# Optimization experiments

Hardware: AMD Instinct MI355X
Metric: run time of the kernel (lower is better)

Reference implementation:

```python
import jax, jax.numpy as jnp
import numpy as np

B, V, E, L, D = 16, 19, 361, 256, 64  # batch, vertices, edges/graph, seq_len, d_model
F_IN = 2 * D + 1  # concat(src_feat, tgt_feat, edge_weight)


def _linear_init(key, fan_in, fan_out):
    bound = 1.0 / np.sqrt(fan_in)
    kw, kb = jax.random.split(key)
    W = jax.random.uniform(kw, (fan_in, fan_out), jnp.float32, -bound, bound)
    b = jax.random.uniform(kb, (fan_out,), jnp.float32, -bound, bound)
    return W, b


def setup_inputs() -> dict:
    key = jax.random.key(0)
    ks = jax.random.split(key, 6)
    hidden_states = jax.random.normal(ks[0], (B * V, L, D), jnp.float32)
    edge_index = jax.random.randint(ks[1], (2, B * E, L), 0, B * V, dtype=jnp.int32)
    edge_weight = jax.random.uniform(ks[2], (B * E, L), jnp.float32)
    W1, b1 = _linear_init(ks[3], F_IN, D)
    W2, b2 = _linear_init(ks[4], D, D // 2)
    W3, b3 = _linear_init(ks[5], D // 2, 1)
    skip_param = jnp.float32(0.25)
    return {"hidden_states": hidden_states, "edge_weight": edge_weight,
            "W1": W1, "b1": b1, "W2": W2, "b2": b2, "W3": W3, "b3": b3,
            "skip_param": skip_param, "edge_index": edge_index}


def reference(hidden_states, edge_weight, W1, b1, W2, b2, W3, b3, skip_param, edge_index):
    # hidden_states: (B*V, L, D) -> (B, L, V, D) for per-timestep node gather
    hs = hidden_states.reshape(B, V, L, D).transpose(0, 2, 1, 3)
    # edge indices are global node ids; local vertex id = idx % V (as in torch code)
    src = (edge_index[0] % V).reshape(B, E, L).transpose(0, 2, 1)  # (B, L, E)
    tgt = (edge_index[1] % V).reshape(B, E, L).transpose(0, 2, 1)
    ew = edge_weight.reshape(B, E, L).transpose(0, 2, 1)           # (B, L, E)
    src_feat = jnp.take_along_axis(hs, src[..., None], axis=2)    # (B, L, E, D)
    tgt_feat = jnp.take_along_axis(hs, tgt[..., None], axis=2)    # (B, L, E, D)
    x = jnp.concatenate([src_feat, tgt_feat, ew[..., None]], axis=-1)  # (B, L, E, 2D+1)
    h = jax.nn.silu(x @ W1 + b1)
    h = jax.nn.silu(h @ W2 + b2)
    w = jax.nn.sigmoid((h @ W3 + b3)[..., 0])                     # (B, L, E)
    new_ew = skip_param * ew + (1.0 - skip_param) * w
    return new_ew.transpose(0, 2, 1).reshape(B * E, L)            # (B*E, L)
```

## Files before the change

### kernel.cpp

```cpp
#include <hip/hip_runtime.h>

#define NB 16
#define NV 19
#define NE 361
#define NL 256
#define ND 64
#define NT 23
#define NEP (NT * 16)
#define ASTRIDE 136

typedef __attribute__((ext_vector_type(8))) short bf16x8;
typedef __attribute__((ext_vector_type(4))) float f32x4;
typedef __attribute__((ext_vector_type(2))) __bf16 bf16v2;

union bf8u { unsigned u[4]; bf16x8 v; uint4 q; };

__device__ __forceinline__ unsigned pack_bf16(float lo, float hi) {
    bf16v2 v; v.x = (__bf16)lo; v.y = (__bf16)hi;
    return __builtin_bit_cast(unsigned, v);
}
__device__ __forceinline__ short f2bf(float f) {
    __bf16 h = (__bf16)f;
    return __builtin_bit_cast(short, h);
}
__device__ __forceinline__ float bflo(unsigned u) {
    return __builtin_bit_cast(float, u << 16);
}
__device__ __forceinline__ float bfhi(unsigned u) {
    return __builtin_bit_cast(float, u & 0xffff0000u);
}
__device__ __forceinline__ f32x4 silu4(f32x4 x) {
    f32x4 t = x * -1.44269504f;
    f32x4 d;
    d.x = __builtin_amdgcn_exp2f(t.x);
    d.y = __builtin_amdgcn_exp2f(t.y);
    d.z = __builtin_amdgcn_exp2f(t.z);
    d.w = __builtin_amdgcn_exp2f(t.w);
    d += 1.f;
    f32x4 r;
    r.x = __builtin_amdgcn_rcpf(d.x);
    r.y = __builtin_amdgcn_rcpf(d.y);
    r.z = __builtin_amdgcn_rcpf(d.z);
    r.w = __builtin_amdgcn_rcpf(d.w);
    return x * r;
}
__device__ __forceinline__ float sigm(float x) {
    return __builtin_amdgcn_rcpf(1.f + __builtin_amdgcn_exp2f(x * -1.44269504f));
}

__global__ __launch_bounds__(256, 4) void edge_learner_kernel(
    const float* __restrict__ hs,
    const float* __restrict__ ew_in,
    const float* __restrict__ W1,
    const float* __restrict__ b1,
    const float* __restrict__ W2,
    const float* __restrict__ b2,
    const float* __restrict__ W3,
    const float* __restrict__ b3,
    const float* __restrict__ skip_p,
    const int*   __restrict__ eidx,
    float* __restrict__ out)
{
    __shared__ __align__(16) short A_s[NV * ASTRIDE];
    __shared__ __align__(16) int4  meta_s[NEP];

    const int tid  = threadIdx.x;
    const int lane = tid & 63;
    const int wave = tid >> 6;
    const int lq   = lane >> 4;
    const int lm   = lane & 15;
    const int bid0 = blockIdx.x;
    const int bid  = (bid0 & 7) * 512 + (bid0 >> 3);
    const int b    = bid >> 8;
    const int l    = bid & 255;

    for (int e = tid; e < NEP; e += 256) {
        int4 m;
        if (e < NE) {
            size_t row = (size_t)(b * NE + e) * NL + l;
            m.x = (eidx[row] % NV) * ASTRIDE;
            m.y = (eidx[(size_t)NB * NE * NL + row] % NV) * ASTRIDE + 64;
            m.z = __builtin_bit_cast(int, ew_in[row]);
            m.w = 0;
        } else {
            m.x = 0; m.y = 64; m.z = 0; m.w = 0;
        }
        meta_s[e] = m;
    }

    f32x4 w1lv[2][2], b1v[2][2];
    #pragma unroll
    for (int ks = 0; ks < 2; ++ks) {
        w1lv[ks][0] = *(const f32x4*)&W1[128 * 64 + ks * 32 + lq * 8];
        w1lv[ks][1] = *(const f32x4*)&W1[128 * 64 + ks * 32 + lq * 8 + 4];
        b1v[ks][0]  = *(const f32x4*)&b1[ks * 32 + lq * 8];
        b1v[ks][1]  = *(const f32x4*)&b1[ks * 32 + lq * 8 + 4];
    }
    bf8u w2f[2][2];
    #pragma unroll
    for (int nt = 0; nt < 2; ++nt)
        #pragma unroll
        for (int ks = 0; ks < 2; ++ks) {
            const float* w2p = &W2[(ks * 32 + lq * 8) * 32 + nt * 16 + lm];
            #pragma unroll
            for (int p = 0; p < 4; ++p)
                w2f[nt][ks].u[p] = pack_bf16(w2p[(2 * p) * 32], w2p[(2 * p + 1) * 32]);
        }
    const f32x4 b2v0 = *(const f32x4*)&b2[lq * 4];
    const f32x4 b2v1 = *(const f32x4*)&b2[16 + lq * 4];
    const f32x4 w3v0 = *(const f32x4*)&W3[lq * 4];
    const f32x4 w3v1 = *(const f32x4*)&W3[16 + lq * 4];
    const float b3v  = b3[0];
    const float skip = skip_p[0];

    {
        const int half = wave >> 1;
        const int oc0  = (wave & 1) * 32;
        bf8u w1f[2][2];
        #pragma unroll
        for (int nt = 0; nt < 2; ++nt)
            #pragma unroll
            for (int ks = 0; ks < 2; ++ks) {
                const float* wp = &W1[(half * 64 + ks * 32 + lq * 8) * 64
                                      + oc0 + nt * 16 + lm];
                #pragma unroll
                for (int p = 0; p < 4; ++p)
                    w1f[nt][ks].u[p] = pack_bf16(wp[(2 * p) * 64], wp[(2 * p + 1) * 64]);
            }

        f32x4 acc00 = {0,0,0,0}, acc01 = {0,0,0,0}, acc10 = {0,0,0,0}, acc11 = {0,0,0,0};
        #pragma unroll
        for (int Mt = 0; Mt < 2; ++Mt) {
            int v  = Mt * 16 + lm;
            int vc = v < NV ? v : NV - 1;
            const float* hp = hs + ((size_t)(b * NV + vc) * NL + l) * ND;
            bf8u af[2];
            #pragma unroll
            for (int ks = 0; ks < 2; ++ks) {
                float4 x0 = *(const float4*)&hp[ks * 32 + lq * 8];
                float4 x1 = *(const float4*)&hp[ks * 32 + lq * 8 + 4];
                af[ks].u[0] = pack_bf16(x0.x, x0.y);
                af[ks].u[1] = pack_bf16(x0.z, x0.w);
                af[ks].u[2] = pack_bf16(x1.x, x1.y);
                af[ks].u[3] = pack_bf16(x1.z, x1.w);
            }
            if (Mt == 0) {
                acc00 = __builtin_amdgcn_mfma_f32_16x16x32_bf16(af[0].v, w1f[0][0].v, acc00, 0, 0, 0);
                acc00 = __builtin_amdgcn_mfma_f32_16x16x32_bf16(af[1].v, w1f[0][1].v, acc00, 0, 0, 0);
                acc01 = __builtin_amdgcn_mfma_f32_16x16x32_bf16(af[0].v, w1f[1][0].v, acc01, 0, 0, 0);
                acc01 = __builtin_amdgcn_mfma_f32_16x16x32_bf16(af[1].v, w1f[1][1].v, acc01, 0, 0, 0);
            } else {
                acc10 = __builtin_amdgcn_mfma_f32_16x16x32_bf16(af[0].v, w1f[0][0].v, acc10, 0, 0, 0);
                acc10 = __builtin_amdgcn_mfma_f32_16x16x32_bf16(af[1].v, w1f[0][1].v, acc10, 0, 0, 0);
                acc11 = __builtin_amdgcn_mfma_f32_16x16x32_bf16(af[0].v, w1f[1][0].v, acc11, 0, 0, 0);
                acc11 = __builtin_amdgcn_mfma_f32_16x16x32_bf16(af[1].v, w1f[1][1].v, acc11, 0, 0, 0);
            }
        }
        #pragma unroll
        for (int r = 0; r < 4; ++r) {
            int v0 = lq * 4 + r;
            A_s[v0 * ASTRIDE + wave * 32 + lm]      = f2bf(acc00[r]);
            A_s[v0 * ASTRIDE + wave * 32 + 16 + lm] = f2bf(acc01[r]);
            int v1 = 16 + lq * 4 + r;
            if (v1 < NV) {
                A_s[v1 * ASTRIDE + wave * 32 + lm]      = f2bf(acc10[r]);
                A_s[v1 * ASTRIDE + wave * 32 + 16 + lm] = f2bf(acc11[r]);
            }
        }
    }
    __syncthreads();

    for (int t = wave; t < NT; t += 4) {
        const int ebase = t * 16;
        const int4 m  = meta_s[ebase + lm];
        const int  so = m.x;
        const int  to = m.y;
        const float ew = __builtin_bit_cast(float, m.z);

        bf8u a1[2];
        #pragma unroll
        for (int ks = 0; ks < 2; ++ks) {
            uint4 as = *(const uint4*)&A_s[so + ks * 32 + lq * 8];
            uint4 at = *(const uint4*)&A_s[to + ks * 32 + lq * 8];
            f32x4 x0, x1;
            x0.x = bflo(as.x) + bflo(at.x);
            x0.y = bfhi(as.x) + bfhi(at.x);
            x0.z = bflo(as.y) + bflo(at.y);
            x0.w = bfhi(as.y) + bfhi(at.y);
            x1.x = bflo(as.z) + bflo(at.z);
            x1.y = bfhi(as.z) + bfhi(at.z);
            x1.z = bflo(as.w) + bflo(at.w);
            x1.w = bfhi(as.w) + bfhi(at.w);
            x0 += b1v[ks][0];  x0 += ew * w1lv[ks][0];
            x1 += b1v[ks][1];  x1 += ew * w1lv[ks][1];
            f32x4 y0 = silu4(x0);
            f32x4 y1 = silu4(x1);
            a1[ks].u[0] = pack_bf16(y0.x, y0.y);
            a1[ks].u[1] = pack_bf16(y0.z, y0.w);
            a1[ks].u[2] = pack_bf16(y1.x, y1.y);
            a1[ks].u[3] = pack_bf16(y1.z, y1.w);
        }

        f32x4 c0 = {0,0,0,0}, c1 = {0,0,0,0};
        c0 = __builtin_amdgcn_mfma_f32_16x16x32_bf16(w2f[0][0].v, a1[0].v, c0, 0, 0, 0);
        c0 = __builtin_amdgcn_mfma_f32_16x16x32_bf16(w2f[0][1].v, a1[1].v, c0, 0, 0, 0);
        c1 = __builtin_amdgcn_mfma_f32_16x16x32_bf16(w2f[1][0].v, a1[0].v, c1, 0, 0, 0);
        c1 = __builtin_amdgcn_mfma_f32_16x16x32_bf16(w2f[1][1].v, a1[1].v, c1, 0, 0, 0);

        f32x4 h0 = silu4(c0 + b2v0);
        f32x4 h1 = silu4(c1 + b2v1);
        f32x4 pv = h0 * w3v0 + h1 * w3v1;
        float p  = (pv.x + pv.y) + (pv.z + pv.w);
        p += __shfl_xor(p, 16);
        p += __shfl_xor(p, 32);

        if (lane < 16) {
            int er = ebase + lane;
            if (er < NE) {
                float wgt = sigm(p + b3v);
                out[(size_t)(b * NE + er) * NL + l] = skip * ew + (1.f - skip) * wgt;
            }
        }
    }
}

extern "C" void kernel_launch(void* const* d_in, const int* in_sizes, int n_in,
                              void* d_out, int out_size, void* d_ws, size_t ws_size,
                              hipStream_t stream) {
    const float* hs   = (const float*)d_in[0];
    const float* ew   = (const float*)d_in[1];
    const float* W1   = (const float*)d_in[2];
    const float* b1   = (const float*)d_in[3];
    const float* W2   = (const float*)d_in[4];
    const float* b2   = (const float*)d_in[5];
    const float* W3   = (const float*)d_in[6];
    const float* b3   = (const float*)d_in[7];
    const float* skip = (const float*)d_in[8];
    const int*   eidx = (const int*)d_in[9];
    float* outp = (float*)d_out;

    dim3 grid(NB * NL);
    dim3 block(256);
    hipLaunchKernelGGL(edge_learner_kernel, grid, block, 0, stream,
                       hs, ew, W1, b1, W2, b2, W3, b3, skip, eidx, outp);
}
```

Before: 58.08 us.

## Fold layer-1 bias into node projections and software-pipeline edge-tile LDS gathers

```diff
diff --git a/kernel.cpp b/kernel.cpp
--- a/kernel.cpp
+++ b/kernel.cpp
@@ -5,8 +5,8 @@
 #define NE 361
 #define NL 256
 #define ND 64
-#define NT 23
-#define NEP (NT * 16)
+#define NTP 24
+#define NEP (NTP * 16)
 #define ASTRIDE 136
 
 typedef __attribute__((ext_vector_type(8))) short bf16x8;
@@ -88,13 +88,11 @@
         meta_s[e] = m;
     }
 
-    f32x4 w1lv[2][2], b1v[2][2];
+    f32x4 w1lv[2][2];
     #pragma unroll
     for (int ks = 0; ks < 2; ++ks) {
         w1lv[ks][0] = *(const f32x4*)&W1[128 * 64 + ks * 32 + lq * 8];
         w1lv[ks][1] = *(const f32x4*)&W1[128 * 64 + ks * 32 + lq * 8 + 4];
-        b1v[ks][0]  = *(const f32x4*)&b1[ks * 32 + lq * 8];
-        b1v[ks][1]  = *(const f32x4*)&b1[ks * 32 + lq * 8 + 4];
     }
     bf8u w2f[2][2];
     #pragma unroll
@@ -116,6 +114,8 @@
     {
         const int half = wave >> 1;
         const int oc0  = (wave & 1) * 32;
+        const float hb0 = 0.5f * b1[(wave * 32 + lm) & 63];
+        const float hb1 = 0.5f * b1[(wave * 32 + 16 + lm) & 63];
         bf8u w1f[2][2];
         #pragma unroll
         for (int nt = 0; nt < 2; ++nt)
@@ -159,29 +159,36 @@
         #pragma unroll
         for (int r = 0; r < 4; ++r) {
             int v0 = lq * 4 + r;
-            A_s[v0 * ASTRIDE + wave * 32 + lm]      = f2bf(acc00[r]);
-            A_s[v0 * ASTRIDE + wave * 32 + 16 + lm] = f2bf(acc01[r]);
+            A_s[v0 * ASTRIDE + wave * 32 + lm]      = f2bf(acc00[r] + hb0);
+            A_s[v0 * ASTRIDE + wave * 32 + 16 + lm] = f2bf(acc01[r] + hb1);
             int v1 = 16 + lq * 4 + r;
             if (v1 < NV) {
-                A_s[v1 * ASTRIDE + wave * 32 + lm]      = f2bf(acc10[r]);
-                A_s[v1 * ASTRIDE + wave * 32 + 16 + lm] = f2bf(acc11[r]);
+                A_s[v1 * ASTRIDE + wave * 32 + lm]      = f2bf(acc10[r] + hb0);
+                A_s[v1 * ASTRIDE + wave * 32 + 16 + lm] = f2bf(acc11[r] + hb1);
             }
         }
     }
     __syncthreads();
 
-    for (int t = wave; t < NT; t += 4) {
-        const int ebase = t * 16;
-        const int4 m  = meta_s[ebase + lm];
-        const int  so = m.x;
-        const int  to = m.y;
-        const float ew = __builtin_bit_cast(float, m.z);
+    int4 mA = meta_s[wave * 16 + lm];
+    uint4 gs0 = *(const uint4*)&A_s[mA.x + lq * 8];
+    uint4 gs1 = *(const uint4*)&A_s[mA.x + 32 + lq * 8];
+    uint4 gt0 = *(const uint4*)&A_s[mA.y + lq * 8];
+    uint4 gt1 = *(const uint4*)&A_s[mA.y + 32 + lq * 8];
+
+    #pragma unroll
+    for (int i = 0; i < 6; ++i) {
+        const int t  = wave + 4 * i;
+        const float ew = __builtin_bit_cast(float, mA.z);
+
+        int4 mB = mA;
+        if (i < 5) mB = meta_s[(t + 4) * 16 + lm];
 
         bf8u a1[2];
         #pragma unroll
         for (int ks = 0; ks < 2; ++ks) {
-            uint4 as = *(const uint4*)&A_s[so + ks * 32 + lq * 8];
-            uint4 at = *(const uint4*)&A_s[to + ks * 32 + lq * 8];
+            const uint4 as = ks ? gs1 : gs0;
+            const uint4 at = ks ? gt1 : gt0;
             f32x4 x0, x1;
             x0.x = bflo(as.x) + bflo(at.x);
             x0.y = bfhi(as.x) + bfhi(at.x);
@@ -191,8 +198,8 @@
             x1.y = bfhi(as.z) + bfhi(at.z);
             x1.z = bflo(as.w) + bflo(at.w);
             x1.w = bfhi(as.w) + bfhi(at.w);
-            x0 += b1v[ks][0];  x0 += ew * w1lv[ks][0];
-            x1 += b1v[ks][1];  x1 += ew * w1lv[ks][1];
+            x0 += ew * w1lv[ks][0];
+            x1 += ew * w1lv[ks][1];
             f32x4 y0 = silu4(x0);
             f32x4 y1 = silu4(x1);
             a1[ks].u[0] = pack_bf16(y0.x, y0.y);
@@ -207,6 +214,14 @@
         c1 = __builtin_amdgcn_mfma_f32_16x16x32_bf16(w2f[1][0].v, a1[0].v, c1, 0, 0, 0);
         c1 = __builtin_amdgcn_mfma_f32_16x16x32_bf16(w2f[1][1].v, a1[1].v, c1, 0, 0, 0);
 
+        uint4 ns0 = gs0, ns1 = gs1, nt0 = gt0, nt1 = gt1;
+        if (i < 5) {
+            ns0 = *(const uint4*)&A_s[mB.x + lq * 8];
+            ns1 = *(const uint4*)&A_s[mB.x + 32 + lq * 8];
+            nt0 = *(const uint4*)&A_s[mB.y + lq * 8];
+            nt1 = *(const uint4*)&A_s[mB.y + 32 + lq * 8];
+        }
+
         f32x4 h0 = silu4(c0 + b2v0);
         f32x4 h1 = silu4(c1 + b2v1);
         f32x4 pv = h0 * w3v0 + h1 * w3v1;
@@ -215,12 +230,15 @@
         p += __shfl_xor(p, 32);
 
         if (lane < 16) {
-            int er = ebase + lane;
+            int er = t * 16 + lane;
             if (er < NE) {
                 float wgt = sigm(p + b3v);
                 out[(size_t)(b * NE + er) * NL + l] = skip * ew + (1.f - skip) * wgt;
             }
         }
+
+        mA = mB;
+        gs0 = ns0; gs1 = ns1; gt0 = nt0; gt1 = nt1;
     }
 }
 
```

Result: no change. 57.51 us (-1.0%).

## Process two timesteps per block and fold half-bias into precomputed node projections

Applied to the files above, without the earlier changes.

```diff
diff --git a/kernel.cpp b/kernel.cpp
--- a/kernel.cpp
+++ b/kernel.cpp
@@ -5,9 +5,10 @@
 #define NE 361
 #define NL 256
 #define ND 64
-#define NT 23
-#define NEP (NT * 16)
+#define NTP 24
+#define NEP (NTP * 16)
 #define ASTRIDE 136
+#define NPAIR 2
 
 typedef __attribute__((ext_vector_type(8))) short bf16x8;
 typedef __attribute__((ext_vector_type(4))) float f32x4;
@@ -61,8 +62,8 @@
     const int*   __restrict__ eidx,
     float* __restrict__ out)
 {
-    __shared__ __align__(16) short A_s[NV * ASTRIDE];
-    __shared__ __align__(16) int4  meta_s[NEP];
+    __shared__ __align__(16) short A_s[NPAIR][NV * ASTRIDE];
+    __shared__ __align__(16) int4  meta_s[NPAIR][NEP];
 
     const int tid  = threadIdx.x;
     const int lane = tid & 63;
@@ -70,14 +71,17 @@
     const int lq   = lane >> 4;
     const int lm   = lane & 15;
     const int bid0 = blockIdx.x;
-    const int bid  = (bid0 & 7) * 512 + (bid0 >> 3);
-    const int b    = bid >> 8;
-    const int l    = bid & 255;
-
-    for (int e = tid; e < NEP; e += 256) {
+    const int bid  = (bid0 & 7) * 256 + (bid0 >> 3);
+    const int plb  = bid * 2;
+    const int b    = plb >> 8;
+    const int l0   = plb & 255;
+
+    for (int i = tid; i < NPAIR * NEP; i += 256) {
+        const int p = (i >= NEP) ? 1 : 0;
+        const int e = i - p * NEP;
         int4 m;
         if (e < NE) {
-            size_t row = (size_t)(b * NE + e) * NL + l;
+            size_t row = (size_t)(b * NE + e) * NL + l0 + p;
             m.x = (eidx[row] % NV) * ASTRIDE;
             m.y = (eidx[(size_t)NB * NE * NL + row] % NV) * ASTRIDE + 64;
             m.z = __builtin_bit_cast(int, ew_in[row]);
@@ -85,16 +89,14 @@
         } else {
             m.x = 0; m.y = 64; m.z = 0; m.w = 0;
         }
-        meta_s[e] = m;
-    }
-
-    f32x4 w1lv[2][2], b1v[2][2];
+        meta_s[p][e] = m;
+    }
+
+    f32x4 w1lv[2][2];
     #pragma unroll
     for (int ks = 0; ks < 2; ++ks) {
         w1lv[ks][0] = *(const f32x4*)&W1[128 * 64 + ks * 32 + lq * 8];
         w1lv[ks][1] = *(const f32x4*)&W1[128 * 64 + ks * 32 + lq * 8 + 4];
-        b1v[ks][0]  = *(const f32x4*)&b1[ks * 32 + lq * 8];
-        b1v[ks][1]  = *(const f32x4*)&b1[ks * 32 + lq * 8 + 4];
     }
     bf8u w2f[2][2];
     #pragma unroll
@@ -116,6 +118,8 @@
     {
         const int half = wave >> 1;
         const int oc0  = (wave & 1) * 32;
+        const float hb0 = 0.5f * b1[(wave * 32 + lm) & 63];
+        const float hb1 = 0.5f * b1[(wave * 32 + 16 + lm) & 63];
         bf8u w1f[2][2];
         #pragma unroll
         for (int nt = 0; nt < 2; ++nt)
@@ -128,97 +132,104 @@
                     w1f[nt][ks].u[p] = pack_bf16(wp[(2 * p) * 64], wp[(2 * p + 1) * 64]);
             }
 
-        f32x4 acc00 = {0,0,0,0}, acc01 = {0,0,0,0}, acc10 = {0,0,0,0}, acc11 = {0,0,0,0};
-        #pragma unroll
-        for (int Mt = 0; Mt < 2; ++Mt) {
-            int v  = Mt * 16 + lm;
-            int vc = v < NV ? v : NV - 1;
-            const float* hp = hs + ((size_t)(b * NV + vc) * NL + l) * ND;
-            bf8u af[2];
+        #pragma unroll
+        for (int p = 0; p < NPAIR; ++p) {
+            f32x4 acc00 = {0,0,0,0}, acc01 = {0,0,0,0},
+                  acc10 = {0,0,0,0}, acc11 = {0,0,0,0};
+            #pragma unroll
+            for (int Mt = 0; Mt < 2; ++Mt) {
+                int v  = Mt * 16 + lm;
+                int vc = v < NV ? v : NV - 1;
+                const float* hp = hs + ((size_t)(b * NV + vc) * NL + l0 + p) * ND;
+                bf8u af[2];
+                #pragma unroll
+                for (int ks = 0; ks < 2; ++ks) {
+                    float4 x0 = *(const float4*)&hp[ks * 32 + lq * 8];
+                    float4 x1 = *(const float4*)&hp[ks * 32 + lq * 8 + 4];
+                    af[ks].u[0] = pack_bf16(x0.x, x0.y);
+                    af[ks].u[1] = pack_bf16(x0.z, x0.w);
+                    af[ks].u[2] = pack_bf16(x1.x, x1.y);
+                    af[ks].u[3] = pack_bf16(x1.z, x1.w);
+                }
+                if (Mt == 0) {
+                    acc00 = __builtin_amdgcn_mfma_f32_16x16x32_bf16(af[0].v, w1f[0][0].v, acc00, 0, 0, 0);
+                    acc00 = __builtin_amdgcn_mfma_f32_16x16x32_bf16(af[1].v, w1f[0][1].v, acc00, 0, 0, 0);
+                    acc01 = __builtin_amdgcn_mfma_f32_16x16x32_bf16(af[0].v, w1f[1][0].v, acc01, 0, 0, 0);
+                    acc01 = __builtin_amdgcn_mfma_f32_16x16x32_bf16(af[1].v, w1f[1][1].v, acc01, 0, 0, 0);
+                } else {
+                    acc10 = __builtin_amdgcn_mfma_f32_16x16x32_bf16(af[0].v, w1f[0][0].v, acc10, 0, 0, 0);
+                    acc10 = __builtin_amdgcn_mfma_f32_16x16x32_bf16(af[1].v, w1f[0][1].v, acc10, 0, 0, 0);
+                    acc11 = __builtin_amdgcn_mfma_f32_16x16x32_bf16(af[0].v, w1f[1][0].v, acc11, 0, 0, 0);
+                    acc11 = __builtin_amdgcn_mfma_f32_16x16x32_bf16(af[1].v, w1f[1][1].v, acc11, 0, 0, 0);
+                }
+            }
+            #pragma unroll
+            for (int r = 0; r < 4; ++r) {
+                int v0 = lq * 4 + r;
+                A_s[p][v0 * ASTRIDE + wave * 32 + lm]      = f2bf(acc00[r] + hb0);
+                A_s[p][v0 * ASTRIDE + wave * 32 + 16 + lm] = f2bf(acc01[r] + hb1);
+                int v1 = 16 + lq * 4 + r;
+                if (v1 < NV) {
+                    A_s[p][v1 * ASTRIDE + wave * 32 + lm]      = f2bf(acc10[r] + hb0);
+                    A_s[p][v1 * ASTRIDE + wave * 32 + 16 + lm] = f2bf(acc11[r] + hb1);
+                }
+            }
+        }
+    }
+    __syncthreads();
+
+    #pragma unroll
+    for (int p = 0; p < NPAIR; ++p) {
+        const short* Ap = A_s[p];
+        const int4*  mp = meta_s[p];
+        float* outp = out + l0 + p;
+
+        #pragma unroll
+        for (int i = 0; i < 6; ++i) {
+            const int t = wave + 4 * i;
+            const int4 m = mp[t * 16 + lm];
+            const int  so = m.x;
+            const int  to = m.y;
+            const float ew = __builtin_bit_cast(float, m.z);
+
+            bf8u a1[2];
             #pragma unroll
             for (int ks = 0; ks < 2; ++ks) {
-                float4 x0 = *(const float4*)&hp[ks * 32 + lq * 8];
-                float4 x1 = *(const float4*)&hp[ks * 32 + lq * 8 + 4];
-                af[ks].u[0] = pack_bf16(x0.x, x0.y);
-                af[ks].u[1] = pack_bf16(x0.z, x0.w);
-                af[ks].u[2] = pack_bf16(x1.x, x1.y);
-                af[ks].u[3] = pack_bf16(x1.z, x1.w);
-            }
-            if (Mt == 0) {
-                acc00 = __builtin_amdgcn_mfma_f32_16x16x32_bf16(af[0].v, w1f[0][0].v, acc00, 0, 0, 0);
-                acc00 = __builtin_amdgcn_mfma_f32_16x16x32_bf16(af[1].v, w1f[0][1].v, acc00, 0, 0, 0);
-                acc01 = __builtin_amdgcn_mfma_f32_16x16x32_bf16(af[0].v, w1f[1][0].v, acc01, 0, 0, 0);
-                acc01 = __builtin_amdgcn_mfma_f32_16x16x32_bf16(af[1].v, w1f[1][1].v, acc01, 0, 0, 0);
-            } else {
-                acc10 = __builtin_amdgcn_mfma_f32_16x16x32_bf16(af[0].v, w1f[0][0].v, acc10, 0, 0, 0);
-                acc10 = __builtin_amdgcn_mfma_f32_16x16x32_bf16(af[1].v, w1f[0][1].v, acc10, 0, 0, 0);
-                acc11 = __builtin_amdgcn_mfma_f32_16x16x32_bf16(af[0].v, w1f[1][0].v, acc11, 0, 0, 0);
-                acc11 = __builtin_amdgcn_mfma_f32_16x16x32_bf16(af[1].v, w1f[1][1].v, acc11, 0, 0, 0);
-            }
-        }
-        #pragma unroll
-        for (int r = 0; r < 4; ++r) {
-            int v0 = lq * 4 + r;
-            A_s[v0 * ASTRIDE + wave * 32 + lm]      = f2bf(acc00[r]);
-            A_s[v0 * ASTRIDE + wave * 32 + 16 + lm] = f2bf(acc01[r]);
-            int v1 = 16 + lq * 4 + r;
-            if (v1 < NV) {
-                A_s[v1 * ASTRIDE + wave * 32 + lm]      = f2bf(acc10[r]);
-                A_s[v1 * ASTRIDE + wave * 32 + 16 + lm] = f2bf(acc11[r]);
-            }
-        }
-    }
-    __syncthreads();
-
-    for (int t = wave; t < NT; t += 4) {
-        const int ebase = t * 16;
-        const int4 m  = meta_s[ebase + lm];
-        const int  so = m.x;
-        const int  to = m.y;
-        const float ew = __builtin_bit_cast(float, m.z);
-
-        bf8u a1[2];
-        #pragma unroll
-        for (int ks = 0; ks < 2; ++ks) {
-            uint4 as = *(const uint4*)&A_s[so + ks * 32 + lq * 8];
-            uint4 at = *(const uint4*)&A_s[to + ks * 32 + lq * 8];
-            f32x4 x0, x1;
-            x0.x = bflo(as.x) + bflo(at.x);
-            x0.y = bfhi(as.x) + bfhi(at.x);
-            x0.z = bflo(as.y) + bflo(at.y);
-            x0.w = bfhi(as.y) + bfhi(at.y);
-            x1.x = bflo(as.z) + bflo(at.z);
-            x1.y = bfhi(as.z) + bfhi(at.z);
-            x1.z = bflo(as.w) + bflo(at.w);
-            x1.w = bfhi(as.w) + bfhi(at.w);
-            x0 += b1v[ks][0];  x0 += ew * w1lv[ks][0];
-            x1 += b1v[ks][1];  x1 += ew * w1lv[ks][1];
-            f32x4 y0 = silu4(x0);
-            f32x4 y1 = silu4(x1);
-            a1[ks].u[0] = pack_bf16(y0.x, y0.y);
-            a1[ks].u[1] = pack_bf16(y0.z, y0.w);
-            a1[ks].u[2] = pack_bf16(y1.x, y1.y);
-            a1[ks].u[3] = pack_bf16(y1.z, y1.w);
-        }
-
-        f32x4 c0 = {0,0,0,0}, c1 = {0,0,0,0};
-        c0 = __builtin_amdgcn_mfma_f32_16x16x32_bf16(w2f[0][0].v, a1[0].v, c0, 0, 0, 0);
-        c0 = __builtin_amdgcn_mfma_f32_16x16x32_bf16(w2f[0][1].v, a1[1].v, c0, 0, 0, 0);
-        c1 = __builtin_amdgcn_mfma_f32_16x16x32_bf16(w2f[1][0].v, a1[0].v, c1, 0, 0, 0);
-        c1 = __builtin_amdgcn_mfma_f32_16x16x32_bf16(w2f[1][1].v, a1[1].v, c1, 0, 0, 0);
-
-        f32x4 h0 = silu4(c0 + b2v0);
-        f32x4 h1 = silu4(c1 + b2v1);
-        f32x4 pv = h0 * w3v0 + h1 * w3v1;
-        float p  = (pv.x + pv.y) + (pv.z + pv.w);
-        p += __shfl_xor(p, 16);
-        p += __shfl_xor(p, 32);
-
-        if (lane < 16) {
-            int er = ebase + lane;
-            if (er < NE) {
-                float wgt = sigm(p + b3v);
-                out[(size_t)(b * NE + er) * NL + l] = skip * ew + (1.f - skip) * wgt;
+                const uint4 as = *(const uint4*)&Ap[so + ks * 32 + lq * 8];
+                const uint4 at = *(const uint4*)&Ap[to + ks * 32 + lq * 8];
+                f32x4 sv0 = { bflo(as.x), bfhi(as.x), bflo(as.y), bfhi(as.y) };
+                f32x4 tv0 = { bflo(at.x), bfhi(at.x), bflo(at.y), bfhi(at.y) };
+                f32x4 sv1 = { bflo(as.z), bfhi(as.z), bflo(as.w), bfhi(as.w) };
+                f32x4 tv1 = { bflo(at.z), bfhi(at.z), bflo(at.w), bfhi(at.w) };
+                f32x4 x0 = sv0 + tv0 + ew * w1lv[ks][0];
+                f32x4 x1 = sv1 + tv1 + ew * w1lv[ks][1];
+                f32x4 y0 = silu4(x0);
+                f32x4 y1 = silu4(x1);
+                a1[ks].u[0] = pack_bf16(y0.x, y0.y);
+                a1[ks].u[1] = pack_bf16(y0.z, y0.w);
+                a1[ks].u[2] = pack_bf16(y1.x, y1.y);
+                a1[ks].u[3] = pack_bf16(y1.z, y1.w);
+            }
+
+            f32x4 c0 = {0,0,0,0}, c1 = {0,0,0,0};
+            c0 = __builtin_amdgcn_mfma_f32_16x16x32_bf16(w2f[0][0].v, a1[0].v, c0, 0, 0, 0);
+            c0 = __builtin_amdgcn_mfma_f32_16x16x32_bf16(w2f[0][1].v, a1[1].v, c0, 0, 0, 0);
+            c1 = __builtin_amdgcn_mfma_f32_16x16x32_bf16(w2f[1][0].v, a1[0].v, c1, 0, 0, 0);
+            c1 = __builtin_amdgcn_mfma_f32_16x16x32_bf16(w2f[1][1].v, a1[1].v, c1, 0, 0, 0);
+
+            f32x4 h0 = silu4(c0 + b2v0);
+            f32x4 h1 = silu4(c1 + b2v1);
+            f32x4 pv = h0 * w3v0 + h1 * w3v1;
+            float pr = (pv.x + pv.y) + (pv.z + pv.w);
+            pr += __shfl_xor(pr, 16);
+            pr += __shfl_xor(pr, 32);
+
+            if (lane < 16) {
+                int er = t * 16 + lane;
+                if (er < NE) {
+                    float wgt = sigm(pr + b3v);
+                    outp[(size_t)(b * NE + er) * NL] = skip * ew + (1.f - skip) * wgt;
+                }
             }
         }
     }
@@ -239,7 +250,7 @@
     const int*   eidx = (const int*)d_in[9];
     float* outp = (float*)d_out;
 
-    dim3 grid(NB * NL);
+    dim3 grid(NB * NL / NPAIR);
     dim3 block(256);
     hipLaunchKernelGGL(edge_learner_kernel, grid, block, 0, stream,
                        hs, ew, W1, b1, W2, b2, W3, b3, skip, eidx, outp);
```

Result: slower. 61.81 us (+6.4%).

## Assign one (batch, timestep) pair per wave and drop block-level sync

Applied to the files above, without the earlier changes.

```diff
diff --git a/kernel.cpp b/kernel.cpp
--- a/kernel.cpp
+++ b/kernel.cpp
@@ -5,8 +5,8 @@
 #define NE 361
 #define NL 256
 #define ND 64
-#define NT 23
-#define NEP (NT * 16)
+#define NTW 23
+#define NEPW (NTW * 16)
 #define ASTRIDE 136
 
 typedef __attribute__((ext_vector_type(8))) short bf16x8;
@@ -61,8 +61,8 @@
     const int*   __restrict__ eidx,
     float* __restrict__ out)
 {
-    __shared__ __align__(16) short A_s[NV * ASTRIDE];
-    __shared__ __align__(16) int4  meta_s[NEP];
+    __shared__ __align__(16) short A_s[4][NV * ASTRIDE];
+    __shared__ __align__(8)  uint2 meta_s[4][NEPW];
 
     const int tid  = threadIdx.x;
     const int lane = tid & 63;
@@ -70,31 +70,33 @@
     const int lq   = lane >> 4;
     const int lm   = lane & 15;
     const int bid0 = blockIdx.x;
-    const int bid  = (bid0 & 7) * 512 + (bid0 >> 3);
-    const int b    = bid >> 8;
-    const int l    = bid & 255;
-
-    for (int e = tid; e < NEP; e += 256) {
-        int4 m;
+    const int bid  = (bid0 & 7) * 128 + (bid0 >> 3);
+    const int pairid = bid * 4 + wave;
+    const int b    = pairid >> 8;
+    const int l    = pairid & 255;
+
+    short*  Aw = A_s[wave];
+    uint2*  Mw = meta_s[wave];
+
+    for (int e = lane; e < NEPW; e += 64) {
+        uint2 m;
         if (e < NE) {
             size_t row = (size_t)(b * NE + e) * NL + l;
-            m.x = (eidx[row] % NV) * ASTRIDE;
-            m.y = (eidx[(size_t)NB * NE * NL + row] % NV) * ASTRIDE + 64;
-            m.z = __builtin_bit_cast(int, ew_in[row]);
-            m.w = 0;
+            unsigned so = (unsigned)((eidx[row] % NV) * ASTRIDE);
+            unsigned to = (unsigned)((eidx[(size_t)NB * NE * NL + row] % NV) * ASTRIDE + 64);
+            m.x = so | (to << 16);
+            m.y = __builtin_bit_cast(unsigned, ew_in[row]);
         } else {
-            m.x = 0; m.y = 64; m.z = 0; m.w = 0;
-        }
-        meta_s[e] = m;
-    }
-
-    f32x4 w1lv[2][2], b1v[2][2];
+            m.x = 64u << 16; m.y = 0u;
+        }
+        Mw[e] = m;
+    }
+
+    f32x4 w1lv[2][2];
     #pragma unroll
     for (int ks = 0; ks < 2; ++ks) {
         w1lv[ks][0] = *(const f32x4*)&W1[128 * 64 + ks * 32 + lq * 8];
         w1lv[ks][1] = *(const f32x4*)&W1[128 * 64 + ks * 32 + lq * 8 + 4];
-        b1v[ks][0]  = *(const f32x4*)&b1[ks * 32 + lq * 8];
-        b1v[ks][1]  = *(const f32x4*)&b1[ks * 32 + lq * 8 + 4];
     }
     bf8u w2f[2][2];
     #pragma unroll
@@ -114,74 +116,73 @@
     const float skip = skip_p[0];
 
     {
-        const int half = wave >> 1;
-        const int oc0  = (wave & 1) * 32;
-        bf8u w1f[2][2];
-        #pragma unroll
-        for (int nt = 0; nt < 2; ++nt)
-            #pragma unroll
-            for (int ks = 0; ks < 2; ++ks) {
-                const float* wp = &W1[(half * 64 + ks * 32 + lq * 8) * 64
-                                      + oc0 + nt * 16 + lm];
-                #pragma unroll
-                for (int p = 0; p < 4; ++p)
-                    w1f[nt][ks].u[p] = pack_bf16(wp[(2 * p) * 64], wp[(2 * p + 1) * 64]);
-            }
-
-        f32x4 acc00 = {0,0,0,0}, acc01 = {0,0,0,0}, acc10 = {0,0,0,0}, acc11 = {0,0,0,0};
+        bf8u af[2][2];
         #pragma unroll
         for (int Mt = 0; Mt < 2; ++Mt) {
             int v  = Mt * 16 + lm;
             int vc = v < NV ? v : NV - 1;
             const float* hp = hs + ((size_t)(b * NV + vc) * NL + l) * ND;
-            bf8u af[2];
             #pragma unroll
             for (int ks = 0; ks < 2; ++ks) {
                 float4 x0 = *(const float4*)&hp[ks * 32 + lq * 8];
                 float4 x1 = *(const float4*)&hp[ks * 32 + lq * 8 + 4];
-                af[ks].u[0] = pack_bf16(x0.x, x0.y);
-                af[ks].u[1] = pack_bf16(x0.z, x0.w);
-                af[ks].u[2] = pack_bf16(x1.x, x1.y);
-                af[ks].u[3] = pack_bf16(x1.z, x1.w);
+                af[Mt][ks].u[0] = pack_bf16(x0.x, x0.y);
+                af[Mt][ks].u[1] = pack_bf16(x0.z, x0.w);
+                af[Mt][ks].u[2] = pack_bf16(x1.x, x1.y);
+                af[Mt][ks].u[3] = pack_bf16(x1.z, x1.w);
             }
-            if (Mt == 0) {
-                acc00 = __builtin_amdgcn_mfma_f32_16x16x32_bf16(af[0].v, w1f[0][0].v, acc00, 0, 0, 0);
-                acc00 = __builtin_amdgcn_mfma_f32_16x16x32_bf16(af[1].v, w1f[0][1].v, acc00, 0, 0, 0);
-                acc01 = __builtin_amdgcn_mfma_f32_16x16x32_bf16(af[0].v, w1f[1][0].v, acc01, 0, 0, 0);
-                acc01 = __builtin_amdgcn_mfma_f32_16x16x32_bf16(af[1].v, w1f[1][1].v, acc01, 0, 0, 0);
-            } else {
-                acc10 = __builtin_amdgcn_mfma_f32_16x16x32_bf16(af[0].v, w1f[0][0].v, acc10, 0, 0, 0);
-                acc10 = __builtin_amdgcn_mfma_f32_16x16x32_bf16(af[1].v, w1f[0][1].v, acc10, 0, 0, 0);
-                acc11 = __builtin_amdgcn_mfma_f32_16x16x32_bf16(af[0].v, w1f[1][0].v, acc11, 0, 0, 0);
-                acc11 = __builtin_amdgcn_mfma_f32_16x16x32_bf16(af[1].v, w1f[1][1].v, acc11, 0, 0, 0);
+        }
+        #pragma unroll
+        for (int cg = 0; cg < 4; ++cg) {
+            const int half = cg >> 1;
+            const int oc0  = (cg & 1) * 32;
+            const float hb0 = 0.5f * b1[(cg * 32 + lm) & 63];
+            const float hb1 = 0.5f * b1[(cg * 32 + 16 + lm) & 63];
+            bf8u w1f[2][2];
+            #pragma unroll
+            for (int nt = 0; nt < 2; ++nt)
+                #pragma unroll
+                for (int ks = 0; ks < 2; ++ks) {
+                    const float* wp = &W1[(half * 64 + ks * 32 + lq * 8) * 64
+                                          + oc0 + nt * 16 + lm];
+                    #pragma unroll
+                    for (int p = 0; p < 4; ++p)
+                        w1f[nt][ks].u[p] = pack_bf16(wp[(2 * p) * 64], wp[(2 * p + 1) * 64]);
+                }
+            f32x4 a00 = {0,0,0,0}, a01 = {0,0,0,0}, a10 = {0,0,0,0}, a11 = {0,0,0,0};
+            a00 = __builtin_amdgcn_mfma_f32_16x16x32_bf16(af[0][0].v, w1f[0][0].v, a00, 0, 0, 0);
+            a00 = __builtin_amdgcn_mfma_f32_16x16x32_bf16(af[0][1].v, w1f[0][1].v, a00, 0, 0, 0);
+            a01 = __builtin_amdgcn_mfma_f32_16x16x32_bf16(af[0][0].v, w1f[1][0].v, a01, 0, 0, 0);
+            a01 = __builtin_amdgcn_mfma_f32_16x16x32_bf16(af[0][1].v, w1f[1][1].v, a01, 0, 0, 0);
+            a10 = __builtin_amdgcn_mfma_f32_16x16x32_bf16(af[1][0].v, w1f[0][0].v, a10, 0, 0, 0);
+            a10 = __builtin_amdgcn_mfma_f32_16x16x32_bf16(af[1][1].v, w1f[0][1].v, a10, 0, 0, 0);
+            a11 = __builtin_amdgcn_mfma_f32_16x16x32_bf16(af[1][0].v, w1f[1][0].v, a11, 0, 0, 0);
+            a11 = __builtin_amdgcn_mfma_f32_16x16x32_bf16(af[1][1].v, w1f[1][1].v, a11, 0, 0, 0);
+            #pragma unroll
+            for (int r = 0; r < 4; ++r) {
+                int v0 = lq * 4 + r;
+                Aw[v0 * ASTRIDE + cg * 32 + lm]      = f2bf(a00[r] + hb0);
+                Aw[v0 * ASTRIDE + cg * 32 + 16 + lm] = f2bf(a01[r] + hb1);
+                int v1 = 16 + lq * 4 + r;
+                if (v1 < NV) {
+                    Aw[v1 * ASTRIDE + cg * 32 + lm]      = f2bf(a10[r] + hb0);
+                    Aw[v1 * ASTRIDE + cg * 32 + 16 + lm] = f2bf(a11[r] + hb1);
+                }
             }
         }
-        #pragma unroll
-        for (int r = 0; r < 4; ++r) {
-            int v0 = lq * 4 + r;
-            A_s[v0 * ASTRIDE + wave * 32 + lm]      = f2bf(acc00[r]);
-            A_s[v0 * ASTRIDE + wave * 32 + 16 + lm] = f2bf(acc01[r]);
-            int v1 = 16 + lq * 4 + r;
-            if (v1 < NV) {
-                A_s[v1 * ASTRIDE + wave * 32 + lm]      = f2bf(acc10[r]);
-                A_s[v1 * ASTRIDE + wave * 32 + 16 + lm] = f2bf(acc11[r]);
-            }
-        }
-    }
-    __syncthreads();
-
-    for (int t = wave; t < NT; t += 4) {
-        const int ebase = t * 16;
-        const int4 m  = meta_s[ebase + lm];
-        const int  so = m.x;
-        const int  to = m.y;
-        const float ew = __builtin_bit_cast(float, m.z);
+    }
+
+    for (int t = 0; t < NTW; ++t) {
+        const uint2 m = Mw[t * 16 + lm];
+        const int so = (int)(m.x & 0xffffu);
+        const int to = (int)(m.x >> 16);
+        const float ew = __builtin_bit_cast(float, m.y);
 
         bf8u a1[2];
         #pragma unroll
         for (int ks = 0; ks < 2; ++ks) {
-            uint4 as = *(const uint4*)&A_s[so + ks * 32 + lq * 8];
-            uint4 at = *(const uint4*)&A_s[to + ks * 32 + lq * 8];
+            const uint4 as = *(const uint4*)&Aw[so + ks * 32 + lq * 8];
+            const uint4 at = *(const uint4*)&Aw[to + ks * 32 + lq * 8];
             f32x4 x0, x1;
             x0.x = bflo(as.x) + bflo(at.x);
             x0.y = bfhi(as.x) + bfhi(at.x);
@@ -191,8 +192,8 @@
             x1.y = bfhi(as.z) + bfhi(at.z);
             x1.z = bflo(as.w) + bflo(at.w);
             x1.w = bfhi(as.w) + bfhi(at.w);
-            x0 += b1v[ks][0];  x0 += ew * w1lv[ks][0];
-            x1 += b1v[ks][1];  x1 += ew * w1lv[ks][1];
+            x0 += ew * w1lv[ks][0];
+            x1 += ew * w1lv[ks][1];
             f32x4 y0 = silu4(x0);
             f32x4 y1 = silu4(x1);
             a1[ks].u[0] = pack_bf16(y0.x, y0.y);
@@ -215,7 +216,7 @@
         p += __shfl_xor(p, 32);
 
         if (lane < 16) {
-            int er = ebase + lane;
+            int er = t * 16 + lane;
             if (er < NE) {
                 float wgt = sigm(p + b3v);
                 out[(size_t)(b * NE + er) * NL + l] = skip * ew + (1.f - skip) * wgt;
@@ -239,7 +240,7 @@
     const int*   eidx = (const int*)d_in[9];
     float* outp = (float*)d_out;
 
-    dim3 grid(NB * NL);
+    dim3 grid(NB * NL / 4);
     dim3 block(256);
     hipLaunchKernelGGL(edge_learner_kernel, grid, block, 0, stream,
                        hs, ew, W1, b1, W2, b2, W3, b3, skip, eidx, outp);
```

New measurement: 68.55 us. 18.0% more time.
